# Kernel tuning notes

Hardware: AMD Instinct MI355X
Metric: run time of the kernel (lower is better)

## Reference

```python
import jax, jax.numpy as jnp
import numpy as np

EPS = 1e-5  # eqx.nn.LayerNorm default


def _layer_norm(x, w, b):
    m = x.mean(-1, keepdims=True)
    v = ((x - m) ** 2).mean(-1, keepdims=True)
    return (x - m) / jnp.sqrt(v + EPS) * w + b


def _s4_block(x, nw, nb, lre, lim, bre, bim, cre, cim, d, lstep, ow, ob, o2w, o2b):
    # x: [L, H]. One SequenceBlock: LayerNorm -> S4 recurrence (lax.scan) -> GELU -> GLU-style gated linear -> residual.
    skip = x
    h = _layer_norm(x, nw, nb)
    Lam = lre + 1j * lim                      # [H, N] complex diagonal state matrix
    step = jnp.exp(lstep)[:, None]            # [H, 1] per-channel timescale
    BL = 1.0 / (1.0 - (step / 2.0) * Lam)     # bilinear discretization
    Abar = BL * (1.0 + (step / 2.0) * Lam)    # [H, N]
    Bbar = BL * step * (bre + 1j * bim)       # [H, N]
    C = cre + 1j * cim                        # [H, N]

    def scan_fn(state, u):                    # state: [H, N] complex, u: [H]
        new = Abar * state + Bbar * u[:, None]
        y = 2.0 * jnp.sum(C * new, axis=-1).real + d * u
        return new, y

    init = jnp.zeros(Abar.shape, Abar.dtype)  # cell.init_state
    _, y = jax.lax.scan(scan_fn, init, h)     # [L, H]
    y = jax.nn.gelu(y)
    y = (y @ ow.T + ob) * jax.nn.sigmoid(y @ o2w.T + o2b)
    return skip + y


def setup_inputs() -> dict:
    key = jax.random.key(0)
    L, IN, OUT, H, N, NL = 2048, 4, 3, 512, 32, 4
    ks = jax.random.split(key, 16)
    return {
        "x": jax.random.normal(ks[0], (L, IN), jnp.float32),
        "enc_w": jax.random.normal(ks[1], (H, IN), jnp.float32) / np.sqrt(IN),
        "enc_b": jnp.zeros((H,), jnp.float32),
        "dec_w": jax.random.normal(ks[2], (OUT, H), jnp.float32) / np.sqrt(H),
        "dec_b": jnp.zeros((OUT,), jnp.float32),
        "norm_w": jnp.ones((NL, H), jnp.float32),
        "norm_b": jnp.zeros((NL, H), jnp.float32),
        "lam_re": -0.5 - jax.random.uniform(ks[3], (NL, H, N), jnp.float32),  # stable (Re < 0)
        "lam_im": np.pi * jax.random.normal(ks[4], (NL, H, N), jnp.float32),
        "b_re": jax.random.normal(ks[5], (NL, H, N), jnp.float32) / np.sqrt(N),
        "b_im": jax.random.normal(ks[6], (NL, H, N), jnp.float32) / np.sqrt(N),
        "c_re": jax.random.normal(ks[7], (NL, H, N), jnp.float32) / np.sqrt(N),
        "c_im": jax.random.normal(ks[8], (NL, H, N), jnp.float32) / np.sqrt(N),
        "d": jax.random.normal(ks[9], (NL, H), jnp.float32),
        "log_step": float(np.log(1e-3)) + float(np.log(1e-1) - np.log(1e-3)) * jax.random.uniform(ks[10], (NL, H), jnp.float32),
        "out_w": jax.random.normal(ks[11], (NL, H, H), jnp.float32) / np.sqrt(H),
        "out_b": jnp.zeros((NL, H), jnp.float32),
        "out2_w": jax.random.normal(ks[12], (NL, H, H), jnp.float32) / np.sqrt(H),
        "out2_b": jnp.zeros((NL, H), jnp.float32),
    }


def reference(x, enc_w, enc_b, dec_w, dec_b, norm_w, norm_b, lam_re, lam_im, b_re, b_im, c_re, c_im, d, log_step, out_w, out_b, out2_w, out2_b):
    h = x @ enc_w.T + enc_b                   # encoder: [L, IN] -> [L, H]
    for i in range(norm_w.shape[0]):          # fixed small n_layers loop
        h = _s4_block(h, norm_w[i], norm_b[i], lam_re[i], lam_im[i], b_re[i], b_im[i],
                      c_re[i], c_im[i], d[i], log_step[i], out_w[i], out_b[i], out2_w[i], out2_b[i])
    return h @ dec_w.T + dec_b                # decoder: [L, H] -> [L, OUT]
```

## Files before the change

### kernel.cpp

```cpp
#include <hip/hip_runtime.h>
#include <hip/hip_bf16.h>
#include <math.h>

#define LSEQ 2048
#define HD   512
#define NST  32
#define LC   32
#define NCHK 64
#define HH   (HD * HD)
#define NTHR 256

typedef __bf16 bf16;
typedef __bf16 bf16x8 __attribute__((ext_vector_type(8)));
typedef float  floatx4 __attribute__((ext_vector_type(4)));

__device__ __forceinline__ float gelu_tanh(float x) {
    float z = 0.7978845608028654f * (x + 0.044715f * x * x * x);
    float e = __expf(2.f * z);
    float th = 1.f - 2.f / (e + 1.f);
    return 0.5f * x * (1.f + th);
}

__device__ __forceinline__ void make_ab(float lre, float lim, float step,
                                        float br0, float bi0,
                                        float& ar, float& ai, float& br, float& bi) {
    float s2 = 0.5f * step;
    float dr = 1.f - s2 * lre, di = -s2 * lim;
    float inv = 1.f / (dr * dr + di * di);
    float blr = dr * inv, bli = -di * inv;
    float nr = 1.f + s2 * lre, ni = s2 * lim;
    ar = blr * nr - bli * ni;
    ai = blr * ni + bli * nr;
    float tr = step * br0, ti = step * bi0;
    br = blr * tr - bli * ti;
    bi = blr * ti + bli * tr;
}

__global__ __launch_bounds__(256) void setup_kernel(
    const float* __restrict__ x,   const float* __restrict__ ew,
    const float* __restrict__ eb,  const float* __restrict__ ow,
    const float* __restrict__ o2w,
    const float* __restrict__ lre, const float* __restrict__ lim,
    const float* __restrict__ bre, const float* __restrict__ bim,
    const float* __restrict__ cre, const float* __restrict__ cim,
    const float* __restrict__ ls,
    float* __restrict__ h, bf16* __restrict__ wb,
    float2* __restrict__ cA, float2* __restrict__ cB,
    float2* __restrict__ cC, float2* __restrict__ cAp,
    float2* __restrict__ statP) {
    int bid = blockIdx.x, tid = threadIdx.x;
    if (bid < 4096) {
        int idx = bid * 256 + tid;
        int t = idx >> 9, col = idx & (HD - 1);
        float4 xv = *(const float4*)(x + t * 4);
        float4 wv = *(const float4*)(ew + col * 4);
        float acc = eb[col];
        acc = fmaf(xv.x, wv.x, acc); acc = fmaf(xv.y, wv.y, acc);
        acc = fmaf(xv.z, wv.z, acc); acc = fmaf(xv.w, wv.w, acc);
        h[idx] = acc;
        float s = acc, s2 = acc * acc;
#pragma unroll
        for (int m = 1; m <= 8; m <<= 1) {
            s  += __shfl_xor(s, m, 64);
            s2 += __shfl_xor(s2, m, 64);
        }
        if ((tid & 15) == 0) statP[(size_t)t * 32 + (col >> 4)] = make_float2(s, s2);
    } else if (bid < 5120) {
        int b2 = bid - 4096;
        const float* src = (b2 >= 512) ? o2w : ow;
        bf16* dst = wb + (b2 >= 512 ? 4 * HH : 0);
        int i = ((b2 & 511) * 256 + tid) * 8;
        float4 a = *(const float4*)(src + i);
        float4 b = *(const float4*)(src + i + 4);
        bf16x8 o;
        o[0] = (bf16)a.x; o[1] = (bf16)a.y; o[2] = (bf16)a.z; o[3] = (bf16)a.w;
        o[4] = (bf16)b.x; o[5] = (bf16)b.y; o[6] = (bf16)b.z; o[7] = (bf16)b.w;
        *(bf16x8*)(dst + i) = o;
    } else {
        int tg = (bid - 5120) * 256 + tid;
        int lay = tg >> 14, rem = tg & 16383;
        int ch = rem >> 5, n = rem & 31;
        float step = __expf(ls[lay * HD + ch]);
        float ar, ai, br, bi;
        make_ab(lre[tg], lim[tg], step, bre[tg], bim[tg], ar, ai, br, bi);
        float xr = ar, xi = ai;
#pragma unroll
        for (int q = 0; q < 5; ++q) { float tt = xr * xr - xi * xi; xi = 2.f * xr * xi; xr = tt; }
        int dst = (lay * NST + n) * HD + ch;
        cA[dst]  = make_float2(ar, ai);
        cB[dst]  = make_float2(br, bi);
        cC[dst]  = make_float2(2.f * cre[tg], 2.f * cim[tg]);
        cAp[dst] = make_float2(xr, xi);
    }
}

__device__ __forceinline__ void stats_and_tile(
    float* tile, float2* stat_s,
    const float* __restrict__ h, const float2* __restrict__ statP,
    const float* __restrict__ nwp, const float* __restrict__ nbp,
    int bx, int by, int tid) {
    if (tid < 128) {
        const float4* pp = (const float4*)(statP + (size_t)(by * 128 + tid) * 32);
        float S = 0.f, S2 = 0.f;
#pragma unroll
        for (int k = 0; k < 16; ++k) {
            float4 v = pp[k];
            S += v.x + v.z; S2 += v.y + v.w;
        }
        float m = S * (1.f / HD);
        float var = S2 * (1.f / HD) - m * m;
        stat_s[tid] = make_float2(m, rsqrtf(var + 1e-5f));
    }
    __syncthreads();
    const float* ub = h + (size_t)(by * 4 * LC) * HD + bx * 16;
    const float* wp = nwp + bx * 16;
    const float* bp = nbp + bx * 16;
#pragma unroll
    for (int r = 0; r < 2; ++r) {
        int i = r * NTHR + tid;
        int tr = i >> 2, c4 = (i & 3) * 4;
        float4 hv = *(const float4*)(ub + (size_t)tr * HD + c4);
        float2 s2 = stat_s[tr];
        float4 gv = *(const float4*)(wp + c4);
        float4 bv = *(const float4*)(bp + c4);
        float4 o;
        o.x = (hv.x - s2.x) * s2.y * gv.x + bv.x;
        o.y = (hv.y - s2.x) * s2.y * gv.y + bv.y;
        o.z = (hv.z - s2.x) * s2.y * gv.z + bv.z;
        o.w = (hv.w - s2.x) * s2.y * gv.w + bv.w;
        *(float4*)(tile + tr * 16 + c4) = o;
    }
}

__global__ __launch_bounds__(256, 2) void p1_kernel(
    const float* __restrict__ h, const float2* __restrict__ statP,
    const float* __restrict__ nwp, const float* __restrict__ nbp,
    const float2* __restrict__ cA, const float2* __restrict__ cB,
    float2* __restrict__ f, int lay) {
    __shared__ float tile[4 * LC * 16];
    __shared__ float2 stat_s[128];
    int tid = threadIdx.x;
    int lane = tid & 63, w = tid >> 6;
    int chl = lane & 15, sub = lane >> 4;
    int bx = blockIdx.x, by = blockIdx.y;
    int ch = bx * 16 + chl;
    int chunk = by * 4 + w;
    stats_and_tile(tile, stat_s, h, statP, nwp, nbp, bx, by, tid);
    int cbase = (lay * NST + sub * 8) * HD + ch;
    float aR[8], aI[8], bR[8], bI[8];
#pragma unroll
    for (int j = 0; j < 8; ++j) {
        float2 t = cA[cbase + j * HD]; aR[j] = t.x; aI[j] = t.y;
        t = cB[cbase + j * HD];        bR[j] = t.x; bI[j] = t.y;
    }
    float sr[8], si[8];
#pragma unroll
    for (int j = 0; j < 8; ++j) { sr[j] = 0.f; si[j] = 0.f; }
    __syncthreads();
    const float* tp = tile + (w * LC) * 16 + chl;
#pragma unroll 4
    for (int t = 0; t < LC; ++t) {
        float uu = tp[t * 16];
#pragma unroll
        for (int j = 0; j < 8; ++j) {
            float nr = fmaf(aR[j], sr[j], fmaf(-aI[j], si[j], bR[j] * uu));
            float ni = fmaf(aI[j], sr[j], fmaf( aR[j], si[j], bI[j] * uu));
            sr[j] = nr; si[j] = ni;
        }
    }
    float2* fp = f + (size_t)(chunk * NST + sub * 8) * HD + ch;
#pragma unroll
    for (int j = 0; j < 8; ++j) fp[(size_t)j * HD] = make_float2(sr[j], si[j]);
}

__global__ __launch_bounds__(256) void p2_kernel(
    float2* __restrict__ f, const float2* __restrict__ cAp, int lay) {
    int tg = blockIdx.x * 256 + threadIdx.x;
    int ch = tg & 511, n = tg >> 9;
    float2 ap = cAp[(lay * NST + n) * HD + ch];
    float2* fp = f + (size_t)n * HD + ch;
    const size_t CS = (size_t)NST * HD;
    float2 cur[8], nxt[8];
#pragma unroll
    for (int k = 0; k < 8; ++k) cur[k] = fp[(size_t)k * CS];
    float sr = 0.f, si = 0.f;
#pragma unroll
    for (int b = 0; b < 8; ++b) {
        if (b < 7) {
#pragma unroll
            for (int k = 0; k < 8; ++k) nxt[k] = fp[(size_t)(b * 8 + 8 + k) * CS];
        }
#pragma unroll
        for (int k = 0; k < 8; ++k) {
            float nr = fmaf(ap.x, sr, fmaf(-ap.y, si, cur[k].x));
            float ni = fmaf(ap.y, sr, fmaf( ap.x, si, cur[k].y));
            sr = nr; si = ni;
            fp[(size_t)(b * 8 + k) * CS] = make_float2(sr, si);
        }
#pragma unroll
        for (int k = 0; k < 8; ++k) cur[k] = nxt[k];
    }
}

__global__ __launch_bounds__(256, 2) void p3_kernel(
    const float* __restrict__ h, const float2* __restrict__ statP,
    const float* __restrict__ nwp, const float* __restrict__ nbp,
    const float2* __restrict__ f,
    const float2* __restrict__ cA, const float2* __restrict__ cB,
    const float2* __restrict__ cC, const float* __restrict__ d_p,
    bf16* __restrict__ g, int lay) {
    __shared__ float tile[4 * LC * 16];
    __shared__ float2 stat_s[128];
    int tid = threadIdx.x;
    int lane = tid & 63, w = tid >> 6;
    int chl = lane & 15, sub = lane >> 4;
    int bx = blockIdx.x, by = blockIdx.y;
    int ch = bx * 16 + chl;
    int chunk = by * 4 + w;
    stats_and_tile(tile, stat_s, h, statP, nwp, nbp, bx, by, tid);
    int cbase = (lay * NST + sub * 8) * HD + ch;
    float aR[8], aI[8], bR[8], bI[8], cR[8], cI[8];
#pragma unroll
    for (int j = 0; j < 8; ++j) {
        float2 t = cA[cbase + j * HD]; aR[j] = t.x; aI[j] = t.y;
        t = cB[cbase + j * HD];        bR[j] = t.x; bI[j] = t.y;
        t = cC[cbase + j * HD];        cR[j] = t.x; cI[j] = t.y;
    }
    float dch = d_p[lay * HD + ch];
    float sr[8], si[8];
    if (chunk > 0) {
        const float2* ip = f + (size_t)((chunk - 1) * NST + sub * 8) * HD + ch;
#pragma unroll
        for (int j = 0; j < 8; ++j) { float2 v = ip[(size_t)j * HD]; sr[j] = v.x; si[j] = v.y; }
    } else {
#pragma unroll
        for (int j = 0; j < 8; ++j) { sr[j] = 0.f; si[j] = 0.f; }
    }
    __syncthreads();
    const float* tp = tile + (w * LC) * 16 + chl;
    bf16* gp = g + (size_t)chunk * LC * HD + ch;
#pragma unroll 4
    for (int t = 0; t < LC; ++t) {
        float uu = tp[t * 16];
        float p = 0.f;
#pragma unroll
        for (int j = 0; j < 8; ++j) {
            float nr = fmaf(aR[j], sr[j], fmaf(-aI[j], si[j], bR[j] * uu));
            float ni = fmaf(aI[j], sr[j], fmaf( aR[j], si[j], bI[j] * uu));
            sr[j] = nr; si[j] = ni;
            p = fmaf(cR[j], nr, fmaf(-cI[j], ni, p));
        }
        p += __shfl_xor(p, 16);
        p += __shfl_xor(p, 32);
        float y = fmaf(dch, uu, p);
        if (sub == 0) gp[(size_t)t * HD] = (bf16)gelu_tanh(y);
    }
}

__global__ __launch_bounds__(256, 2) void mm_kernel(
    const bf16* __restrict__ A,
    const bf16* __restrict__ W1,
    const bf16* __restrict__ W2,
    const float* __restrict__ bias1, const float* __restrict__ bias2,
    float* __restrict__ Hio, float2* __restrict__ statP, int doStats) {
    const int w = threadIdx.x >> 6, lane = threadIdx.x & 63;
    const int wm = w >> 1, wn = w & 1;
    const int bm = blockIdx.x >> 4, bn = blockIdx.x & 15;
    const int mW = bm * 64 + wm * 32;
    const int nW = bn * 32 + wn * 16;
    const int lrow = lane & 15, quad = lane >> 4;

    floatx4 acc1[2] = {{0.f,0.f,0.f,0.f},{0.f,0.f,0.f,0.f}};
    floatx4 acc2[2] = {{0.f,0.f,0.f,0.f},{0.f,0.f,0.f,0.f}};
    for (int k0 = 0; k0 < HD; k0 += 32) {
        int kk = k0 + quad * 8;
        bf16x8 a0 = *(const bf16x8*)(A + (size_t)(mW + lrow) * HD + kk);
        bf16x8 a1 = *(const bf16x8*)(A + (size_t)(mW + 16 + lrow) * HD + kk);
        bf16x8 p0 = *(const bf16x8*)(W1 + (size_t)(nW + lrow) * HD + kk);
        bf16x8 q0 = *(const bf16x8*)(W2 + (size_t)(nW + lrow) * HD + kk);
        acc1[0] = __builtin_amdgcn_mfma_f32_16x16x32_bf16(a0, p0, acc1[0], 0, 0, 0);
        acc1[1] = __builtin_amdgcn_mfma_f32_16x16x32_bf16(a1, p0, acc1[1], 0, 0, 0);
        acc2[0] = __builtin_amdgcn_mfma_f32_16x16x32_bf16(a0, q0, acc2[0], 0, 0, 0);
        acc2[1] = __builtin_amdgcn_mfma_f32_16x16x32_bf16(a1, q0, acc2[1], 0, 0, 0);
    }
    int jj = nW + lrow;
    float bb1 = bias1[jj], bb2 = bias2[jj];
    float hn_[2][4];
#pragma unroll
    for (int fm = 0; fm < 2; ++fm)
#pragma unroll
        for (int r = 0; r < 4; ++r) {
            int t = mW + fm * 16 + quad * 4 + r;
            float z1 = acc1[fm][r] + bb1;
            float z2 = acc2[fm][r] + bb2;
            float v = Hio[(size_t)t * HD + jj] + z1 / (1.f + __expf(-z2));
            Hio[(size_t)t * HD + jj] = v;
            hn_[fm][r] = v;
        }
    if (doStats) {
#pragma unroll
        for (int fm = 0; fm < 2; ++fm)
#pragma unroll
            for (int r = 0; r < 4; ++r) {
                float s = hn_[fm][r], s2 = s * s;
#pragma unroll
                for (int m = 1; m <= 8; m <<= 1) {
                    s  += __shfl_xor(s, m, 64);
                    s2 += __shfl_xor(s2, m, 64);
                }
                if (lrow == 0) {
                    int t = mW + fm * 16 + quad * 4 + r;
                    statP[(size_t)t * 32 + (nW >> 4)] = make_float2(s, s2);
                }
            }
    }
}

__global__ __launch_bounds__(192) void dec_kernel(
    const float* __restrict__ h, const float* __restrict__ w,
    const float* __restrict__ b, float* __restrict__ out) {
    int j = threadIdx.x >> 6, lane = threadIdx.x & 63;
    int t = blockIdx.x;
    const float* hp = h + (size_t)t * HD + lane * 8;
    float v[8];
    *(float4*)(v)     = *(const float4*)(hp);
    *(float4*)(v + 4) = *(const float4*)(hp + 4);
    float w8[8];
    *(float4*)(w8)     = *(const float4*)(w + j * HD + lane * 8);
    *(float4*)(w8 + 4) = *(const float4*)(w + j * HD + lane * 8 + 4);
    float s = 0.f;
#pragma unroll
    for (int e = 0; e < 8; ++e) s = fmaf(v[e], w8[e], s);
#pragma unroll
    for (int m = 32; m; m >>= 1) s += __shfl_xor(s, m, 64);
    if (lane == 0) out[t * 3 + j] = s + b[j];
}

extern "C" void kernel_launch(void* const* d_in, const int* in_sizes, int n_in,
                              void* d_out, int out_size, void* d_ws, size_t ws_size,
                              hipStream_t stream) {
    const float* x   = (const float*)d_in[0];
    const float* ew  = (const float*)d_in[1];
    const float* eb  = (const float*)d_in[2];
    const float* dw  = (const float*)d_in[3];
    const float* db  = (const float*)d_in[4];
    const float* nw  = (const float*)d_in[5];
    const float* nb  = (const float*)d_in[6];
    const float* lre = (const float*)d_in[7];
    const float* lim = (const float*)d_in[8];
    const float* bre = (const float*)d_in[9];
    const float* bim = (const float*)d_in[10];
    const float* cre = (const float*)d_in[11];
    const float* cim = (const float*)d_in[12];
    const float* dd  = (const float*)d_in[13];
    const float* ls  = (const float*)d_in[14];
    const float* ow  = (const float*)d_in[15];
    const float* ob  = (const float*)d_in[16];
    const float* o2w = (const float*)d_in[17];
    const float* o2b = (const float*)d_in[18];

    char* ws = (char*)d_ws;
    float*  h     = (float*)ws;
    float2* f     = (float2*)(ws + (4  << 20));
    bf16*   g     = (bf16*)(ws + (16 << 20));
    bf16*   wb    = (bf16*)(ws + (18 << 20));
    float2* cA    = (float2*)(ws + (22 << 20));
    float2* cB    = (float2*)(ws + (22 << 20) + (512 << 10));
    float2* cC    = (float2*)(ws + (23 << 20));
    float2* cAp   = (float2*)(ws + (23 << 20) + (512 << 10));
    float2* statP = (float2*)(ws + (24 << 20));

    setup_kernel<<<5376, 256, 0, stream>>>(x, ew, eb, ow, o2w,
                                           lre, lim, bre, bim, cre, cim, ls,
                                           h, wb, cA, cB, cC, cAp, statP);
    for (int lay = 0; lay < 4; ++lay) {
        int oH = lay * HD;
        p1_kernel<<<dim3(HD / 16, NCHK / 4), 256, 0, stream>>>(
            h, statP, nw + oH, nb + oH, cA, cB, f, lay);
        p2_kernel<<<64, 256, 0, stream>>>(f, cAp, lay);
        p3_kernel<<<dim3(HD / 16, NCHK / 4), 256, 0, stream>>>(
            h, statP, nw + oH, nb + oH, f, cA, cB, cC, dd, g, lay);
        mm_kernel<<<512, 256, 0, stream>>>(
            g, wb + lay * HH, wb + 4 * HH + lay * HH, ob + oH, o2b + oH, h,
            statP, lay < 3 ? 1 : 0);
    }
    dec_kernel<<<LSEQ, 192, 0, stream>>>(h, dw, db, (float*)d_out);
}
```

Measured before the change: 305.4 us.

## Make chunked S4 scan hierarchical: in-block superchunk scan, short cross-superchunk scan

The sequential 64-step carry scan in p2 becomes a two-level scan. p1 now scans 8 chunks per block in shared memory and writes local prefix states. p2 scans only 8 superchunk totals using A^(8*LC) powers. p3 rebuilds each chunk's initial state from the local prefix, the superchunk carry and precomputed powers of A (cApJ) built in setup. LayerNorm is also folded into the scan loop through per-row stats instead of a separate normalize pass. This shortens p2's serial chain at the cost of extra loads in p3 and a 512-thread p1 with a lower block count.

```diff
diff --git a/kernel.cpp b/kernel.cpp
--- a/kernel.cpp
+++ b/kernel.cpp
@@ -7,8 +7,8 @@
 #define NST  32
 #define LC   32
 #define NCHK 64
+#define NSUP 8
 #define HH   (HD * HD)
-#define NTHR 256
 
 typedef __bf16 bf16;
 typedef __bf16 bf16x8 __attribute__((ext_vector_type(8)));
@@ -47,7 +47,7 @@
     float* __restrict__ h, bf16* __restrict__ wb,
     float2* __restrict__ cA, float2* __restrict__ cB,
     float2* __restrict__ cC, float2* __restrict__ cAp,
-    float2* __restrict__ statP) {
+    float2* __restrict__ cApJ, float2* __restrict__ statP) {
     int bid = blockIdx.x, tid = threadIdx.x;
     if (bid < 4096) {
         int idx = bid * 256 + tid;
@@ -91,16 +91,41 @@
         cB[dst]  = make_float2(br, bi);
         cC[dst]  = make_float2(2.f * cre[tg], 2.f * cim[tg]);
         cAp[dst] = make_float2(xr, xi);
-    }
-}
-
-__device__ __forceinline__ void stats_and_tile(
-    float* tile, float2* stat_s,
+        float pr = xr, pi = xi;
+#pragma unroll
+        for (int jj = 0; jj < 7; ++jj) {
+            cApJ[((size_t)(lay * 7 + jj) * NST + n) * HD + ch] = make_float2(pr, pi);
+            float t2r = pr * xr - pi * xi;
+            float t2i = pr * xi + pi * xr;
+            pr = t2r; pi = t2i;
+        }
+    }
+}
+
+__global__ __launch_bounds__(512, 1) void p1_kernel(
     const float* __restrict__ h, const float2* __restrict__ statP,
     const float* __restrict__ nwp, const float* __restrict__ nbp,
-    int bx, int by, int tid) {
-    if (tid < 128) {
-        const float4* pp = (const float4*)(statP + (size_t)(by * 128 + tid) * 32);
+    const float2* __restrict__ cA, const float2* __restrict__ cB,
+    const float2* __restrict__ cAp,
+    float2* __restrict__ f, int lay) {
+    __shared__ float tile[256 * 16];
+    __shared__ float2 stat_s[256];
+    __shared__ float2 fs[8 * 32 * 16];
+    const int tid = threadIdx.x;
+    const int lane = tid & 63, w = tid >> 6;
+    const int chl = lane & 15, sub = lane >> 4;
+    const int bx = blockIdx.x, sup = blockIdx.y;
+    const int ch = bx * 16 + chl;
+
+    const float* ub = h + (size_t)(sup * 256) * HD + bx * 16;
+#pragma unroll
+    for (int r = 0; r < 2; ++r) {
+        int i = r * 512 + tid;
+        int tr = i >> 2, c4 = (i & 3) * 4;
+        *(float4*)(tile + tr * 16 + c4) = *(const float4*)(ub + (size_t)tr * HD + c4);
+    }
+    if (tid < 256) {
+        const float4* pp = (const float4*)(statP + (size_t)(sup * 256 + tid) * 32);
         float S = 0.f, S2 = 0.f;
 #pragma unroll
         for (int k = 0; k < 16; ++k) {
@@ -111,56 +136,26 @@
         float var = S2 * (1.f / HD) - m * m;
         stat_s[tid] = make_float2(m, rsqrtf(var + 1e-5f));
     }
-    __syncthreads();
-    const float* ub = h + (size_t)(by * 4 * LC) * HD + bx * 16;
-    const float* wp = nwp + bx * 16;
-    const float* bp = nbp + bx * 16;
-#pragma unroll
-    for (int r = 0; r < 2; ++r) {
-        int i = r * NTHR + tid;
-        int tr = i >> 2, c4 = (i & 3) * 4;
-        float4 hv = *(const float4*)(ub + (size_t)tr * HD + c4);
-        float2 s2 = stat_s[tr];
-        float4 gv = *(const float4*)(wp + c4);
-        float4 bv = *(const float4*)(bp + c4);
-        float4 o;
-        o.x = (hv.x - s2.x) * s2.y * gv.x + bv.x;
-        o.y = (hv.y - s2.x) * s2.y * gv.y + bv.y;
-        o.z = (hv.z - s2.x) * s2.y * gv.z + bv.z;
-        o.w = (hv.w - s2.x) * s2.y * gv.w + bv.w;
-        *(float4*)(tile + tr * 16 + c4) = o;
-    }
-}
-
-__global__ __launch_bounds__(256, 2) void p1_kernel(
-    const float* __restrict__ h, const float2* __restrict__ statP,
-    const float* __restrict__ nwp, const float* __restrict__ nbp,
-    const float2* __restrict__ cA, const float2* __restrict__ cB,
-    float2* __restrict__ f, int lay) {
-    __shared__ float tile[4 * LC * 16];
-    __shared__ float2 stat_s[128];
-    int tid = threadIdx.x;
-    int lane = tid & 63, w = tid >> 6;
-    int chl = lane & 15, sub = lane >> 4;
-    int bx = blockIdx.x, by = blockIdx.y;
-    int ch = bx * 16 + chl;
-    int chunk = by * 4 + w;
-    stats_and_tile(tile, stat_s, h, statP, nwp, nbp, bx, by, tid);
     int cbase = (lay * NST + sub * 8) * HD + ch;
     float aR[8], aI[8], bR[8], bI[8];
 #pragma unroll
     for (int j = 0; j < 8; ++j) {
-        float2 t = cA[cbase + j * HD]; aR[j] = t.x; aI[j] = t.y;
-        t = cB[cbase + j * HD];        bR[j] = t.x; bI[j] = t.y;
-    }
+        float2 t2 = cA[cbase + j * HD]; aR[j] = t2.x; aI[j] = t2.y;
+        t2 = cB[cbase + j * HD];        bR[j] = t2.x; bI[j] = t2.y;
+    }
+    float gam = nwp[ch], bet = nbp[ch];
+    __syncthreads();
+
+    const float* tp = tile + (w * 32) * 16 + chl;
     float sr[8], si[8];
 #pragma unroll
     for (int j = 0; j < 8; ++j) { sr[j] = 0.f; si[j] = 0.f; }
-    __syncthreads();
-    const float* tp = tile + (w * LC) * 16 + chl;
 #pragma unroll 4
     for (int t = 0; t < LC; ++t) {
-        float uu = tp[t * 16];
+        float2 st = stat_s[w * 32 + t];
+        float gr = gam * st.y;
+        float off = fmaf(-st.x, gr, bet);
+        float uu = fmaf(tp[t * 16], gr, off);
 #pragma unroll
         for (int j = 0; j < 8; ++j) {
             float nr = fmaf(aR[j], sr[j], fmaf(-aI[j], si[j], bR[j] * uu));
@@ -168,80 +163,131 @@
             sr[j] = nr; si[j] = ni;
         }
     }
-    float2* fp = f + (size_t)(chunk * NST + sub * 8) * HD + ch;
-#pragma unroll
-    for (int j = 0; j < 8; ++j) fp[(size_t)j * HD] = make_float2(sr[j], si[j]);
+#pragma unroll
+    for (int j = 0; j < 8; ++j)
+        fs[(w * 32 + sub * 8 + j) * 16 + chl] = make_float2(sr[j], si[j]);
+    __syncthreads();
+
+    int n2 = tid >> 4, c2 = tid & 15;
+    int chg = bx * 16 + c2;
+    float2 ap = cAp[(lay * NST + n2) * HD + chg];
+    const size_t CS = (size_t)NST * HD;
+    float2* fo = f + (size_t)n2 * HD + chg;
+    float s2r = 0.f, s2i = 0.f;
+#pragma unroll
+    for (int k = 0; k < 8; ++k) {
+        float2 v = fs[(k * 32 + n2) * 16 + c2];
+        float nr = fmaf(ap.x, s2r, fmaf(-ap.y, s2i, v.x));
+        float ni = fmaf(ap.y, s2r, fmaf( ap.x, s2i, v.y));
+        s2r = nr; s2i = ni;
+        fo[(size_t)(sup * 8 + k) * CS] = make_float2(s2r, s2i);
+    }
 }
 
 __global__ __launch_bounds__(256) void p2_kernel(
-    float2* __restrict__ f, const float2* __restrict__ cAp, int lay) {
+    const float2* __restrict__ f, const float2* __restrict__ cAp,
+    float2* __restrict__ Sx, int lay) {
     int tg = blockIdx.x * 256 + threadIdx.x;
     int ch = tg & 511, n = tg >> 9;
     float2 ap = cAp[(lay * NST + n) * HD + ch];
-    float2* fp = f + (size_t)n * HD + ch;
+    float xr = ap.x, xi = ap.y;
+#pragma unroll
+    for (int q = 0; q < 3; ++q) { float tt = xr * xr - xi * xi; xi = 2.f * xr * xi; xr = tt; }
     const size_t CS = (size_t)NST * HD;
-    float2 cur[8], nxt[8];
-#pragma unroll
-    for (int k = 0; k < 8; ++k) cur[k] = fp[(size_t)k * CS];
+    const float2* fp = f + (size_t)n * HD + ch;
+    float2 F[8];
+#pragma unroll
+    for (int k = 0; k < 8; ++k) F[k] = fp[(size_t)(k * 8 + 7) * CS];
+    float2* sp = Sx + (size_t)n * HD + ch;
     float sr = 0.f, si = 0.f;
 #pragma unroll
-    for (int b = 0; b < 8; ++b) {
-        if (b < 7) {
-#pragma unroll
-            for (int k = 0; k < 8; ++k) nxt[k] = fp[(size_t)(b * 8 + 8 + k) * CS];
-        }
-#pragma unroll
-        for (int k = 0; k < 8; ++k) {
-            float nr = fmaf(ap.x, sr, fmaf(-ap.y, si, cur[k].x));
-            float ni = fmaf(ap.y, sr, fmaf( ap.x, si, cur[k].y));
-            sr = nr; si = ni;
-            fp[(size_t)(b * 8 + k) * CS] = make_float2(sr, si);
-        }
-#pragma unroll
-        for (int k = 0; k < 8; ++k) cur[k] = nxt[k];
+    for (int k = 0; k < 8; ++k) {
+        sp[(size_t)k * CS] = make_float2(sr, si);
+        float nr = fmaf(xr, sr, fmaf(-xi, si, F[k].x));
+        float ni = fmaf(xi, sr, fmaf( xr, si, F[k].y));
+        sr = nr; si = ni;
     }
 }
 
 __global__ __launch_bounds__(256, 2) void p3_kernel(
     const float* __restrict__ h, const float2* __restrict__ statP,
     const float* __restrict__ nwp, const float* __restrict__ nbp,
-    const float2* __restrict__ f,
+    const float2* __restrict__ f, const float2* __restrict__ Sx,
+    const float2* __restrict__ cApJ,
     const float2* __restrict__ cA, const float2* __restrict__ cB,
     const float2* __restrict__ cC, const float* __restrict__ d_p,
     bf16* __restrict__ g, int lay) {
-    __shared__ float tile[4 * LC * 16];
+    __shared__ float tile[128 * 16];
     __shared__ float2 stat_s[128];
-    int tid = threadIdx.x;
-    int lane = tid & 63, w = tid >> 6;
-    int chl = lane & 15, sub = lane >> 4;
-    int bx = blockIdx.x, by = blockIdx.y;
-    int ch = bx * 16 + chl;
-    int chunk = by * 4 + w;
-    stats_and_tile(tile, stat_s, h, statP, nwp, nbp, bx, by, tid);
+    const int tid = threadIdx.x;
+    const int lane = tid & 63, w = tid >> 6;
+    const int chl = lane & 15, sub = lane >> 4;
+    const int bx = blockIdx.x, by = blockIdx.y;
+    const int ch = bx * 16 + chl;
+    const int chunk = by * 4 + w;
+
+    const float* ub = h + (size_t)(by * 128) * HD + bx * 16;
+#pragma unroll
+    for (int r = 0; r < 2; ++r) {
+        int i = r * 256 + tid;
+        int tr = i >> 2, c4 = (i & 3) * 4;
+        *(float4*)(tile + tr * 16 + c4) = *(const float4*)(ub + (size_t)tr * HD + c4);
+    }
+    if (tid < 128) {
+        const float4* pp = (const float4*)(statP + (size_t)(by * 128 + tid) * 32);
+        float S = 0.f, S2 = 0.f;
+#pragma unroll
+        for (int k = 0; k < 16; ++k) {
+            float4 v = pp[k];
+            S += v.x + v.z; S2 += v.y + v.w;
+        }
+        float m = S * (1.f / HD);
+        float var = S2 * (1.f / HD) - m * m;
+        stat_s[tid] = make_float2(m, rsqrtf(var + 1e-5f));
+    }
     int cbase = (lay * NST + sub * 8) * HD + ch;
     float aR[8], aI[8], bR[8], bI[8], cR[8], cI[8];
 #pragma unroll
     for (int j = 0; j < 8; ++j) {
-        float2 t = cA[cbase + j * HD]; aR[j] = t.x; aI[j] = t.y;
-        t = cB[cbase + j * HD];        bR[j] = t.x; bI[j] = t.y;
-        t = cC[cbase + j * HD];        cR[j] = t.x; cI[j] = t.y;
+        float2 t2 = cA[cbase + j * HD]; aR[j] = t2.x; aI[j] = t2.y;
+        t2 = cB[cbase + j * HD];        bR[j] = t2.x; bI[j] = t2.y;
+        t2 = cC[cbase + j * HD];        cR[j] = t2.x; cI[j] = t2.y;
     }
     float dch = d_p[lay * HD + ch];
+    float gam = nwp[ch], bet = nbp[ch];
+
     float sr[8], si[8];
-    if (chunk > 0) {
-        const float2* ip = f + (size_t)((chunk - 1) * NST + sub * 8) * HD + ch;
-#pragma unroll
-        for (int j = 0; j < 8; ++j) { float2 v = ip[(size_t)j * HD]; sr[j] = v.x; si[j] = v.y; }
+    int jj = chunk & 7, ksup = chunk >> 3;
+    if (chunk == 0) {
+#pragma unroll
+        for (int j = 0; j < 8; ++j) { sr[j] = 0.f; si[j] = 0.f; }
+    } else if (jj == 0) {
+        const float2* sp = Sx + ((size_t)ksup * NST + sub * 8) * HD + ch;
+#pragma unroll
+        for (int j = 0; j < 8; ++j) { float2 v = sp[(size_t)j * HD]; sr[j] = v.x; si[j] = v.y; }
     } else {
-#pragma unroll
-        for (int j = 0; j < 8; ++j) { sr[j] = 0.f; si[j] = 0.f; }
+        const float2* fw = f + ((size_t)(chunk - 1) * NST + sub * 8) * HD + ch;
+        const float2* sp = Sx + ((size_t)ksup * NST + sub * 8) * HD + ch;
+        const float2* aj = cApJ + ((size_t)(lay * 7 + (jj - 1)) * NST + sub * 8) * HD + ch;
+#pragma unroll
+        for (int j = 0; j < 8; ++j) {
+            float2 F = fw[(size_t)j * HD];
+            float2 S = sp[(size_t)j * HD];
+            float2 A = aj[(size_t)j * HD];
+            sr[j] = fmaf(A.x, S.x, fmaf(-A.y, S.y, F.x));
+            si[j] = fmaf(A.x, S.y, fmaf( A.y, S.x, F.y));
+        }
     }
     __syncthreads();
-    const float* tp = tile + (w * LC) * 16 + chl;
+
+    const float* tp = tile + (w * 32) * 16 + chl;
     bf16* gp = g + (size_t)chunk * LC * HD + ch;
 #pragma unroll 4
     for (int t = 0; t < LC; ++t) {
-        float uu = tp[t * 16];
+        float2 st = stat_s[w * 32 + t];
+        float gr = gam * st.y;
+        float off = fmaf(-st.x, gr, bet);
+        float uu = fmaf(tp[t * 16], gr, off);
         float p = 0.f;
 #pragma unroll
         for (int j = 0; j < 8; ++j) {
@@ -369,17 +415,19 @@
     float2* cC    = (float2*)(ws + (23 << 20));
     float2* cAp   = (float2*)(ws + (23 << 20) + (512 << 10));
     float2* statP = (float2*)(ws + (24 << 20));
+    float2* cApJ  = (float2*)(ws + (25 << 20));
+    float2* Sx    = (float2*)(ws + (29 << 20));
 
     setup_kernel<<<5376, 256, 0, stream>>>(x, ew, eb, ow, o2w,
                                            lre, lim, bre, bim, cre, cim, ls,
-                                           h, wb, cA, cB, cC, cAp, statP);
+                                           h, wb, cA, cB, cC, cAp, cApJ, statP);
     for (int lay = 0; lay < 4; ++lay) {
         int oH = lay * HD;
-        p1_kernel<<<dim3(HD / 16, NCHK / 4), 256, 0, stream>>>(
-            h, statP, nw + oH, nb + oH, cA, cB, f, lay);
-        p2_kernel<<<64, 256, 0, stream>>>(f, cAp, lay);
+        p1_kernel<<<dim3(HD / 16, NSUP), 512, 0, stream>>>(
+            h, statP, nw + oH, nb + oH, cA, cB, cAp, f, lay);
+        p2_kernel<<<64, 256, 0, stream>>>(f, cAp, Sx, lay);
         p3_kernel<<<dim3(HD / 16, NCHK / 4), 256, 0, stream>>>(
-            h, statP, nw + oH, nb + oH, f, cA, cB, cC, dd, g, lay);
+            h, statP, nw + oH, nb + oH, f, Sx, cApJ, cA, cB, cC, dd, g, lay);
         mm_kernel<<<512, 256, 0, stream>>>(
             g, wb + lay * HH, wb + 4 * HH + lay * HH, ob + oH, o2b + oH, h,
             statP, lay < 3 ? 1 : 0);
```

Result: no change. 308.3 us (+0.9%).
